# Optimization experiments

Measured on AMD Instinct MI355X. Metric: run time of the kernel, lower is better.

Reference implementation:

```python
import jax, jax.numpy as jnp
import numpy as np

BSZ, L, H, P = 4, 4096, 1024, 512
DT_MIN, DT_MAX = 1e-3, 1e-1


def setup_inputs() -> dict:
    key = jax.random.key(0)
    ks = jax.random.split(key, 6)
    input_sequence = jax.random.normal(ks[0], (BSZ, 1, H, 1, L), jnp.float32)
    # hidden_state_method='zero': hiddens arg only has to carry the right shape
    hiddens = jnp.zeros((BSZ, 1, P), jnp.float32)
    # stable (left-half-plane) diagonal state matrix, like HiPPO-LegS eigenvalues
    Lambda_re = -0.5 * jax.random.uniform(ks[1], (P,), jnp.float32) - 0.1
    Lambda_im = jnp.pi * jnp.arange(P, dtype=jnp.float32)
    # B stored as (P, H, 2) real/imag pair (lecun-ish scale), C as (H, P, 2)
    B = jax.random.normal(ks[2], (P, H, 2), jnp.float32) / jnp.sqrt(2.0 * H)
    C = jax.random.normal(ks[3], (H, P, 2), jnp.float32) / jnp.sqrt(2.0 * P)
    D = jax.random.normal(ks[4], (H,), jnp.float32)
    log_step = jax.random.uniform(ks[5], (P, 1), jnp.float32,
                                  minval=float(np.log(DT_MIN)),
                                  maxval=float(np.log(DT_MAX)))
    return dict(input_sequence=input_sequence, hiddens=hiddens,
                Lambda_re=Lambda_re, Lambda_im=Lambda_im,
                B=B, C=C, D=D, log_step=log_step)


def _binop(qi, qj):
    # diagonal linear recurrence combine: x_j = A_j * x_i + b_j
    Ai, bi = qi
    Aj, bj = qj
    return (Aj * Ai, Aj * bi + bj)


def _s5_forward(input_sequence, Lambda_re, Lambda_im, B, C, D, log_step):
    Lam = jax.lax.complex(Lambda_re, Lambda_im)              # (P,)
    step = jnp.exp(log_step[:, 0])                           # (P,)
    # zero-order-hold discretization
    Lambda_bar = jnp.exp(Lam * step)                         # (P,) complex
    B_scale = (Lambda_bar - 1.0) / Lam                       # (P,) complex
    B_bar_re = B_scale.real[:, None] * B[..., 0] - B_scale.imag[:, None] * B[..., 1]
    B_bar_im = B_scale.real[:, None] * B[..., 1] + B_scale.imag[:, None] * B[..., 0]

    u = input_sequence[:, 0, :, 0].transpose(0, 2, 1)        # (BSZ, L, H) float32

    # Bu_t = B_bar @ u_t, done on real/imag parts to keep u real in the GEMM
    Bu = jax.lax.complex(jnp.einsum('blh,ph->blp', u, B_bar_re),
                         jnp.einsum('blh,ph->blp', u, B_bar_im))  # (BSZ,L,P)
    # prepend zero hidden state (hidden_state_method='zero')
    zeros0 = jnp.zeros((Bu.shape[0], 1, Bu.shape[2]), Bu.dtype)
    Bu_elems = jnp.concatenate([zeros0, Bu], axis=1)          # (BSZ,L+1,P)
    Lam_elems = jnp.broadcast_to(Lambda_bar, Bu_elems.shape)  # (BSZ,L+1,P)

    _, xs = jax.lax.associative_scan(_binop, (Lam_elems, Bu_elems), axis=1)
    xs = xs[:, 1:]                                            # (BSZ,L,P) complex states

    # conj_sym=True: y_t = 2 * Re(C_tilde @ x_t)
    Cr, Ci = C[..., 0], C[..., 1]                             # (H,P) each
    ys = 2.0 * (jnp.einsum('hp,blp->blh', Cr, xs.real)
                - jnp.einsum('hp,blp->blh', Ci, xs.imag))     # (BSZ,L,H)
    ys = ys + D * u                                           # feedthrough
    ys = jax.nn.gelu(ys, approximate=False)                   # activation='gelu'
    return ys.transpose(0, 2, 1)[:, None, :, None, :]         # (BSZ,1,H,1,L)


def reference(input_sequence, hiddens, Lambda_re, Lambda_im, B, C, D, log_step):
    del hiddens  # unused with hidden_state_method='zero'
    return _s5_forward(input_sequence, Lambda_re, Lambda_im, B, C, D, log_step)
```

## Files before the change

### kernel.cpp

```cpp
#include <hip/hip_runtime.h>
#include <math.h>


constexpr int kB = 4, kL = 4096, kH = 1024, kP = 512;
constexpr int kM = 1024, kK = 1024, kN = 4096;

typedef short bf16x8 __attribute__((ext_vector_type(8)));
typedef float f32x4 __attribute__((ext_vector_type(4)));

constexpr size_t A1H_OFF = 0;
constexpr size_t A2H_OFF = A1H_OFF + (size_t)kM * kK * 2;
constexpr size_t LBAR_B  = A2H_OFF + (size_t)kM * kK * 2;
constexpr size_t BU_B    = (LBAR_B + 4096 + 255) & ~(size_t)255;
constexpr size_t TH_B    = BU_B + (size_t)kB * kM * kN * 4;
constexpr size_t MID_BYTES = TH_B + (size_t)kB * kN * kK * 2;

__device__ __forceinline__ unsigned short f2bf(float x) {
  unsigned int u = __float_as_uint(x);
  u += 0x7fffu + ((u >> 16) & 1u);
  return (unsigned short)(u >> 16);
}
__device__ __forceinline__ float bf2f(unsigned short h) {
  return __uint_as_float(((unsigned int)h) << 16);
}

__device__ __forceinline__ void gl2lds16(const void* g, void* l) {
  __builtin_amdgcn_global_load_lds(
      (const __attribute__((address_space(1))) void*)g,
      (__attribute__((address_space(3))) void*)l, 16, 0, 0);
}

template <int N>
__device__ __forceinline__ void wait_vm() {
  __builtin_amdgcn_s_waitcnt((N & 15) | ((N >> 4) << 14) | (15 << 8) | (7 << 4));
}

__global__ __launch_bounds__(256) void k_prep1(
    const float* __restrict__ Lre, const float* __restrict__ Lim,
    const float* __restrict__ B, const float* __restrict__ log_step,
    unsigned char* __restrict__ ws) {
  int p = blockIdx.x;
  float lr = Lre[p], li = Lim[p];
  float step = expf(log_step[p]);
  float er = expf(lr * step);
  float sb, cb;
  sincosf(li * step, &sb, &cb);
  float lbr = er * cb, lbi = er * sb;
  float nr = lbr - 1.0f, ni = lbi;
  float inv = 1.0f / (lr * lr + li * li);
  float sr = (nr * lr + ni * li) * inv;
  float si = (ni * lr - nr * li) * inv;

  if (threadIdx.x == 0) ((float2*)(ws + LBAR_B))[p] = make_float2(lbr, lbi);

  unsigned short* a1h = (unsigned short*)(ws + A1H_OFF);
  const float* Brow = B + (size_t)p * kH * 2;
  for (int h = threadIdx.x; h < kH; h += 256) {
    float br = Brow[2 * h], bi = Brow[2 * h + 1];
    a1h[(size_t)p * kK + h] = f2bf(sr * br - si * bi);
    a1h[(size_t)(kP + p) * kK + h] = f2bf(sr * bi + si * br);
  }
}

__global__ __launch_bounds__(256) void k_prep2(
    const float* __restrict__ C, unsigned char* __restrict__ ws) {
  int h = blockIdx.x;
  unsigned short* a2h = (unsigned short*)(ws + A2H_OFF);
  for (int k = threadIdx.x; k < kK; k += 256) {
    float v = (k < kP) ? 2.f * C[((size_t)h * kP + k) * 2]
                       : -2.f * C[((size_t)h * kP + (k - kP)) * 2 + 1];
    a2h[(size_t)h * kK + k] = f2bf(v);
  }
}

__global__ __launch_bounds__(256) void k_transpose(
    const float* __restrict__ in, unsigned short* __restrict__ oh) {
  __shared__ float t[64][65];
  int b = blockIdx.z;
  int r0 = blockIdx.y * 64;
  int c0 = blockIdx.x * 64;
  int tid = threadIdx.x;
  const float* src = in + ((size_t)b * 1024 + r0) * 4096 + c0;
  int cc = (tid & 15) * 4, rr = tid >> 4;
#pragma unroll
  for (int i = 0; i < 4; i++) {
    float4 v = *(const float4*)(src + (size_t)(rr + i * 16) * 4096 + cc);
    t[rr + i * 16][cc + 0] = v.x;
    t[rr + i * 16][cc + 1] = v.y;
    t[rr + i * 16][cc + 2] = v.z;
    t[rr + i * 16][cc + 3] = v.w;
  }
  __syncthreads();
  int oc = tid >> 2;
  int og = (tid & 3) * 2;
#pragma unroll
  for (int i = 0; i < 2; i++) {
    int g = og + i;
    unsigned short hv[8];
#pragma unroll
    for (int j = 0; j < 8; j++) hv[j] = f2bf(t[g * 8 + j][oc]);
    size_t ob = ((size_t)b * 4096 + c0 + oc) * 1024 + r0 + g * 8;
    *(uint4*)(oh + ob) = *(uint4*)hv;
  }
}


__device__ __forceinline__ int stage_src_off(int Dp) {
  int Ds = Dp ^ (((Dp >> 9) & 1) << 5);
  int s = Ds >> 10, d = Ds & 1023;
  int row = ((s >> 1) << 4) + (d >> 6);
  int kk = ((s & 1) << 5) + ((d & 63) >> 1);
  return row * kK + kk;
}

__device__ __forceinline__ void stg_half(const unsigned short* p, int h, int kt,
                                         unsigned char* lds, int lbase,
                                         int rowk0, int rowk1, int d0, int d1) {
  const unsigned short* s = p + (size_t)h * (128 * kK) + kt * 64;
  gl2lds16(s + rowk0, lds + lbase + h * 16384 + d0);
  gl2lds16(s + rowk1, lds + lbase + h * 16384 + d1);
}

template <int MH>
__device__ __forceinline__ void rd_ah(bf16x8 (&a)[4][2], const unsigned char* lds,
                                      int base, int wmrb, int lane_off) {
#pragma unroll
  for (int mi = 0; mi < 4; mi++)
#pragma unroll
    for (int ks = 0; ks < 2; ks++)
      a[mi][ks] = *(const bf16x8*)(lds + base +
          (((wmrb + MH * 4 + mi) * 2 + ks) << 10) + lane_off);
}
template <int NH>
__device__ __forceinline__ void rd_bh(bf16x8 (&bb)[2][2][2], const unsigned char* lds,
                                      int base, int wnrb, int lane_off) {
#pragma unroll
  for (int nj = 0; nj < 2; nj++)
#pragma unroll
    for (int ks = 0; ks < 2; ks++)
      bb[NH][nj][ks] = *(const bf16x8*)(lds + base +
          (((wnrb + NH * 2 + nj) * 2 + ks) << 10) + lane_off);
}

template <int MH, int NH>
__device__ __forceinline__ void mfma_quad(f32x4 (&acc)[8][4], bf16x8 (&a)[4][2],
                                          bf16x8 (&bb)[2][2][2]) {
  __builtin_amdgcn_s_setprio(1);
#pragma unroll
  for (int ks = 0; ks < 2; ks++)
#pragma unroll
    for (int mi = 0; mi < 4; mi++)
#pragma unroll
      for (int nj = 0; nj < 2; nj++)
        acc[MH * 4 + mi][NH * 2 + nj] = __builtin_amdgcn_mfma_f32_16x16x32_bf16(
            a[mi][ks], bb[NH][nj][ks], acc[MH * 4 + mi][NH * 2 + nj], 0, 0, 0);
  __builtin_amdgcn_s_setprio(0);
}

#define BAR __builtin_amdgcn_s_barrier()
#define LGKM0                                           \
  do {                                                  \
    asm volatile("s_waitcnt lgkmcnt(0)" ::: "memory");  \
    __builtin_amdgcn_sched_barrier(0);                  \
  } while (0)

template <bool EPI>
__global__ __launch_bounds__(512) void k_gemm8(
    const unsigned short* __restrict__ Ah, const unsigned short* __restrict__ Bh,
    float* __restrict__ out, const float* __restrict__ u,
    const float* __restrict__ D) {
  __shared__ __align__(16) unsigned char lds[131072];
  constexpr int LA0 = 0, LA1 = 32768, LB0 = 65536, LB1 = 98304;
  constexpr int NT2 = kK / 128;

  int b = blockIdx.z;
  int m0 = blockIdx.y * 256, n0 = blockIdx.x * 256;
  int tid = threadIdx.x, w = tid >> 6;
  int q = (tid >> 4) & 3, r = tid & 15;
  int wm = (w >> 2) * 128, wn = (w & 3) * 64;
  int wmrb = (w >> 2) * 8, wnrb = (w & 3) * 4;
  int lane_off = (r * 64 + q * 16) ^ ((r & 8) << 2);

  int d0 = tid << 4, d1 = 8192 + (tid << 4);
  int rowk0 = stage_src_off(d0), rowk1 = stage_src_off(d1);

  const unsigned short* pA = Ah + (size_t)m0 * kK;
  const unsigned short* pB = Bh + (size_t)b * kN * kK + (size_t)n0 * kK;

  f32x4 acc[8][4] = {};
  bf16x8 a[4][2], bb[2][2][2];

#define STG(P, H, KT, LB) stg_half(P, H, KT, lds, LB, rowk0, rowk1, d0, d1)

  STG(pA, 0, 0, LA0); STG(pA, 1, 0, LA0);
  STG(pB, 0, 0, LB0); STG(pB, 1, 0, LB0);
  STG(pB, 0, 1, LB1); STG(pB, 1, 1, LB1);
  wait_vm<4>();
  BAR;

  for (int it = 0; it < NT2; ++it) {
    int kt = it * 2;
    bool pf = (it + 1 < NT2);
    rd_ah<0>(a, lds, LA0, wmrb, lane_off);
    rd_bh<0>(bb, lds, LB0, wnrb, lane_off);
    STG(pA, 0, kt + 1, LA1);
    BAR; LGKM0; mfma_quad<0, 0>(acc, a, bb); BAR;
    rd_bh<1>(bb, lds, LB0, wnrb, lane_off);
    STG(pA, 1, kt + 1, LA1);
    BAR; LGKM0; mfma_quad<0, 1>(acc, a, bb); BAR;
    rd_ah<1>(a, lds, LA0, wmrb, lane_off);
    if (pf) STG(pB, 0, kt + 2, LB0);
    BAR; LGKM0; mfma_quad<1, 1>(acc, a, bb); BAR;
    if (pf) STG(pB, 1, kt + 2, LB0);
    BAR; mfma_quad<1, 0>(acc, a, bb);
    if (pf) wait_vm<4>(); else wait_vm<0>();
    BAR;
    rd_ah<0>(a, lds, LA1, wmrb, lane_off);
    rd_bh<0>(bb, lds, LB1, wnrb, lane_off);
    if (pf) STG(pA, 0, kt + 2, LA0);
    BAR; LGKM0; mfma_quad<0, 0>(acc, a, bb); BAR;
    rd_bh<1>(bb, lds, LB1, wnrb, lane_off);
    if (pf) STG(pA, 1, kt + 2, LA0);
    BAR; LGKM0; mfma_quad<0, 1>(acc, a, bb); BAR;
    rd_ah<1>(a, lds, LA1, wmrb, lane_off);
    if (pf) STG(pB, 0, kt + 3, LB1);
    BAR; LGKM0; mfma_quad<1, 1>(acc, a, bb); BAR;
    if (pf) STG(pB, 1, kt + 3, LB1);
    BAR; mfma_quad<1, 0>(acc, a, bb);
    if (pf) wait_vm<4>();
    BAR;
  }
#undef STG

#pragma unroll
  for (int mi = 0; mi < 8; mi++) {
#pragma unroll
    for (int reg = 0; reg < 4; reg++) {
      int row = m0 + wm + mi * 16 + q * 4 + reg;
      float dv = EPI ? D[row] : 0.f;
#pragma unroll
      for (int ni = 0; ni < 4; ni++) {
        int col = n0 + wn + ni * 16 + r;
        size_t o = ((size_t)b * kM + row) * (size_t)kN + col;
        float v = acc[mi][ni][reg];
        if (EPI) {
          float y = v + dv * u[o];
          v = 0.5f * y * (1.f + erff(y * 0.70710678118654752f));
        }
        out[o] = v;
      }
    }
  }
}

__global__ __launch_bounds__(256) void k_scan(float* __restrict__ bu,
                                              const float2* __restrict__ lbar) {
  int p = blockIdx.x & (kP - 1);
  int b = blockIdx.x >> 9;
  int tid = threadIdx.x, lane = tid & 63, w = tid >> 6;
  float2 lam = lbar[p];
  float* sre = bu + ((size_t)b * kM + p) * (size_t)kN;
  float* sim = sre + (size_t)kP * kN;

  float vr[16], vi[16];
  {
    const float4* pr = (const float4*)(sre + tid * 16);
    const float4* pi = (const float4*)(sim + tid * 16);
#pragma unroll
    for (int i = 0; i < 4; i++) {
      float4 a = pr[i], c = pi[i];
      vr[4 * i] = a.x; vr[4 * i + 1] = a.y; vr[4 * i + 2] = a.z; vr[4 * i + 3] = a.w;
      vi[4 * i] = c.x; vi[4 * i + 1] = c.y; vi[4 * i + 2] = c.z; vi[4 * i + 3] = c.w;
    }
  }

  float xr = 0.f, xi = 0.f;
#pragma unroll
  for (int i = 0; i < 16; i++) {
    float nr2 = fmaf(lam.x, xr, fmaf(-lam.y, xi, vr[i]));
    float ni2 = fmaf(lam.x, xi, fmaf(lam.y, xr, vi[i]));
    xr = nr2; xi = ni2;
  }

  float Ar = lam.x, Ai = lam.y;
#pragma unroll
  for (int s = 0; s < 4; s++) {
    float tr = Ar * Ar - Ai * Ai, ti = 2.f * Ar * Ai;
    Ar = tr; Ai = ti;
  }
  float br = xr, bi = xi;

  for (int off = 1; off < 64; off <<= 1) {
    float pAr = __shfl_up(Ar, off), pAi = __shfl_up(Ai, off);
    float pbr = __shfl_up(br, off), pbi = __shfl_up(bi, off);
    if (lane >= off) {
      float nAr = Ar * pAr - Ai * pAi;
      float nAi = Ar * pAi + Ai * pAr;
      float nbr = Ar * pbr - Ai * pbi + br;
      float nbi = Ar * pbi + Ai * pbr + bi;
      Ar = nAr; Ai = nAi; br = nbr; bi = nbi;
    }
  }

  __shared__ float4 wtot[4];
  if (lane == 63) wtot[w] = make_float4(Ar, Ai, br, bi);
  __syncthreads();

  float eAr = __shfl_up(Ar, 1), eAi = __shfl_up(Ai, 1);
  float ebr = __shfl_up(br, 1), ebi = __shfl_up(bi, 1);
  if (lane == 0) { eAr = 1.f; eAi = 0.f; ebr = 0.f; ebi = 0.f; }

  float pAr = 1.f, pAi = 0.f, pbr = 0.f, pbi = 0.f;
  for (int j = 0; j < w; j++) {
    float4 t = wtot[j];
    float nAr = t.x * pAr - t.y * pAi;
    float nAi = t.x * pAi + t.y * pAr;
    float nbr = t.x * pbr - t.y * pbi + t.z;
    float nbi = t.x * pbi + t.y * pbr + t.w;
    pAr = nAr; pAi = nAi; pbr = nbr; pbi = nbi;
  }

  float initr = eAr * pbr - eAi * pbi + ebr;
  float initi = eAr * pbi + eAi * pbr + ebi;

  xr = initr; xi = initi;
  float4* qr = (float4*)(sre + tid * 16);
  float4* qi = (float4*)(sim + tid * 16);
#pragma unroll
  for (int i = 0; i < 4; i++) {
    float rr[4], ii[4];
#pragma unroll
    for (int j = 0; j < 4; j++) {
      float nr2 = fmaf(lam.x, xr, fmaf(-lam.y, xi, vr[4 * i + j]));
      float ni2 = fmaf(lam.x, xi, fmaf(lam.y, xr, vi[4 * i + j]));
      xr = nr2; xi = ni2; rr[j] = nr2; ii[j] = ni2;
    }
    qr[i] = make_float4(rr[0], rr[1], rr[2], rr[3]);
    qi[i] = make_float4(ii[0], ii[1], ii[2], ii[3]);
  }
}

constexpr size_t OBBAR = 0;
constexpr size_t OLBAR = (size_t)kP * kH;
constexpr size_t OBU = OLBAR + 1024;

__global__ __launch_bounds__(256) void k_precomputeF(
    const float* __restrict__ Lre, const float* __restrict__ Lim,
    const float* __restrict__ B, const float* __restrict__ log_step,
    float2* __restrict__ ws) {
  int p = blockIdx.x;
  float lr = Lre[p], li = Lim[p];
  float step = expf(log_step[p]);
  float er = expf(lr * step);
  float sb, cb;
  sincosf(li * step, &sb, &cb);
  float lbr = er * cb, lbi = er * sb;
  float nr = lbr - 1.0f, ni = lbi;
  float inv = 1.0f / (lr * lr + li * li);
  float sr = (nr * lr + ni * li) * inv;
  float si = (ni * lr - nr * li) * inv;
  if (threadIdx.x == 0) ws[OLBAR + p] = make_float2(lbr, lbi);
  float2* Bbar = ws + OBBAR;
  const float* Brow = B + (size_t)p * kH * 2;
  for (int h = threadIdx.x; h < kH; h += 256) {
    float br = Brow[2 * h], bi = Brow[2 * h + 1];
    Bbar[(size_t)p * kH + h] = make_float2(sr * br - si * bi, sr * bi + si * br);
  }
}

__global__ __launch_bounds__(256) void k_gemm1F(
    const float2* __restrict__ ws_bbar, const float* __restrict__ u,
    float2* __restrict__ Bu) {
  __shared__ float2 As[16][64];
  __shared__ float Bs[16][64];
  int b = blockIdx.z, m0 = blockIdx.y * 64, n0 = blockIdx.x * 64;
  int tid = threadIdx.x, tn = tid & 15, tm = tid >> 4;
  const float* uB = u + (size_t)b * kH * kL;
  float2 acc[4][4];
#pragma unroll
  for (int i = 0; i < 4; i++)
#pragma unroll
    for (int j = 0; j < 4; j++) acc[i][j] = make_float2(0.f, 0.f);
  int ar = tid >> 2, ac = (tid & 3) * 4, bk = tid >> 4, bc = (tid & 15) * 4;
  for (int k0 = 0; k0 < kH; k0 += 16) {
    const float4* src = (const float4*)(ws_bbar + (size_t)(m0 + ar) * kH + k0 + ac);
    float4 v01 = src[0], v23 = src[1];
    As[ac + 0][ar] = make_float2(v01.x, v01.y);
    As[ac + 1][ar] = make_float2(v01.z, v01.w);
    As[ac + 2][ar] = make_float2(v23.x, v23.y);
    As[ac + 3][ar] = make_float2(v23.z, v23.w);
    float4 v = *(const float4*)(uB + (size_t)(k0 + bk) * kL + n0 + bc);
    *(float4*)&Bs[bk][bc] = v;
    __syncthreads();
#pragma unroll
    for (int kk = 0; kk < 16; ++kk) {
      const float4* arow = (const float4*)&As[kk][0];
      float4 a01 = arow[tm * 2 + 0], a23 = arow[tm * 2 + 1];
      float2 a[4] = {make_float2(a01.x, a01.y), make_float2(a01.z, a01.w),
                     make_float2(a23.x, a23.y), make_float2(a23.z, a23.w)};
      float4 bv = ((const float4*)&Bs[kk][0])[tn];
      float bbv[4] = {bv.x, bv.y, bv.z, bv.w};
#pragma unroll
      for (int mi = 0; mi < 4; mi++)
#pragma unroll
        for (int ni = 0; ni < 4; ni++) {
          acc[mi][ni].x = fmaf(a[mi].x, bbv[ni], acc[mi][ni].x);
          acc[mi][ni].y = fmaf(a[mi].y, bbv[ni], acc[mi][ni].y);
        }
    }
    __syncthreads();
  }
  float2* BuB = Bu + (size_t)b * kP * kL;
#pragma unroll
  for (int mi = 0; mi < 4; mi++) {
    int row = m0 + tm * 4 + mi;
    float2* dst = BuB + (size_t)row * kL + n0 + tn * 4;
    ((float4*)dst)[0] = make_float4(acc[mi][0].x, acc[mi][0].y, acc[mi][1].x, acc[mi][1].y);
    ((float4*)dst)[1] = make_float4(acc[mi][2].x, acc[mi][2].y, acc[mi][3].x, acc[mi][3].y);
  }
}

__global__ __launch_bounds__(256) void k_scanF(float2* __restrict__ Bu,
                                               const float2* __restrict__ Lbar) {
  int p = blockIdx.x & (kP - 1);
  int b = blockIdx.x >> 9;
  int tid = threadIdx.x, lane = tid & 63, w = tid >> 6;
  float2 lam = Lbar[p];
  float2* seq = Bu + ((size_t)b * kP + p) * kL;
  float2 v[16];
  const float4* src = (const float4*)(seq + tid * 16);
#pragma unroll
  for (int i = 0; i < 8; i++) {
    float4 t = src[i];
    v[2 * i] = make_float2(t.x, t.y);
    v[2 * i + 1] = make_float2(t.z, t.w);
  }
  float xr = 0.f, xi = 0.f;
#pragma unroll
  for (int i = 0; i < 16; i++) {
    float nr2 = fmaf(lam.x, xr, fmaf(-lam.y, xi, v[i].x));
    float ni2 = fmaf(lam.x, xi, fmaf(lam.y, xr, v[i].y));
    xr = nr2; xi = ni2;
  }
  float Ar = lam.x, Ai = lam.y;
#pragma unroll
  for (int s = 0; s < 4; s++) {
    float tr = Ar * Ar - Ai * Ai, ti = 2.f * Ar * Ai;
    Ar = tr; Ai = ti;
  }
  float br = xr, bi = xi;
  for (int off = 1; off < 64; off <<= 1) {
    float pAr = __shfl_up(Ar, off), pAi = __shfl_up(Ai, off);
    float pbr = __shfl_up(br, off), pbi = __shfl_up(bi, off);
    if (lane >= off) {
      float nAr = Ar * pAr - Ai * pAi, nAi = Ar * pAi + Ai * pAr;
      float nbr = Ar * pbr - Ai * pbi + br, nbi = Ar * pbi + Ai * pbr + bi;
      Ar = nAr; Ai = nAi; br = nbr; bi = nbi;
    }
  }
  __shared__ float4 wtot[4];
  if (lane == 63) wtot[w] = make_float4(Ar, Ai, br, bi);
  __syncthreads();
  float eAr = __shfl_up(Ar, 1), eAi = __shfl_up(Ai, 1);
  float ebr = __shfl_up(br, 1), ebi = __shfl_up(bi, 1);
  if (lane == 0) { eAr = 1.f; eAi = 0.f; ebr = 0.f; ebi = 0.f; }
  float pAr = 1.f, pAi = 0.f, pbr = 0.f, pbi = 0.f;
  for (int j = 0; j < w; j++) {
    float4 t = wtot[j];
    float nAr = t.x * pAr - t.y * pAi, nAi = t.x * pAi + t.y * pAr;
    float nbr = t.x * pbr - t.y * pbi + t.z, nbi = t.x * pbi + t.y * pbr + t.w;
    pAr = nAr; pAi = nAi; pbr = nbr; pbi = nbi;
  }
  float initr = eAr * pbr - eAi * pbi + ebr;
  float initi = eAr * pbi + eAi * pbr + ebi;
  xr = initr; xi = initi;
  float4* dst = (float4*)(seq + tid * 16);
#pragma unroll
  for (int i = 0; i < 8; i++) {
    float nr0 = fmaf(lam.x, xr, fmaf(-lam.y, xi, v[2 * i].x));
    float ni0 = fmaf(lam.x, xi, fmaf(lam.y, xr, v[2 * i].y));
    float nr1 = fmaf(lam.x, nr0, fmaf(-lam.y, ni0, v[2 * i + 1].x));
    float ni1 = fmaf(lam.x, ni0, fmaf(lam.y, nr0, v[2 * i + 1].y));
    dst[i] = make_float4(nr0, ni0, nr1, ni1);
    xr = nr1; xi = ni1;
  }
}

__global__ __launch_bounds__(256) void k_gemm2F(
    const float2* __restrict__ C, const float2* __restrict__ X,
    const float* __restrict__ u, const float* __restrict__ D,
    float* __restrict__ out) {
  __shared__ float2 As[16][64];
  __shared__ float2 Bs[16][64];
  int b = blockIdx.z, m0 = blockIdx.y * 64, n0 = blockIdx.x * 64;
  int tid = threadIdx.x, tn = tid & 15, tm = tid >> 4;
  const float2* Xb = X + (size_t)b * kP * kL;
  float acc[4][4];
#pragma unroll
  for (int i = 0; i < 4; i++)
#pragma unroll
    for (int j = 0; j < 4; j++) acc[i][j] = 0.f;
  int ar = tid >> 2, ac = (tid & 3) * 4, bk = tid >> 4, bc = (tid & 15) * 4;
  for (int k0 = 0; k0 < kP; k0 += 16) {
    const float4* src = (const float4*)(C + (size_t)(m0 + ar) * kP + k0 + ac);
    float4 v01 = src[0], v23 = src[1];
    As[ac + 0][ar] = make_float2(v01.x, v01.y);
    As[ac + 1][ar] = make_float2(v01.z, v01.w);
    As[ac + 2][ar] = make_float2(v23.x, v23.y);
    As[ac + 3][ar] = make_float2(v23.z, v23.w);
    const float4* srcb = (const float4*)(Xb + (size_t)(k0 + bk) * kL + n0 + bc);
    ((float4*)&Bs[bk][bc])[0] = srcb[0];
    ((float4*)&Bs[bk][bc])[1] = srcb[1];
    __syncthreads();
#pragma unroll
    for (int kk = 0; kk < 16; ++kk) {
      const float4* arow = (const float4*)&As[kk][0];
      float4 a01 = arow[tm * 2 + 0], a23 = arow[tm * 2 + 1];
      float2 a[4] = {make_float2(a01.x, a01.y), make_float2(a01.z, a01.w),
                     make_float2(a23.x, a23.y), make_float2(a23.z, a23.w)};
      const float4* brow = (const float4*)&Bs[kk][0];
      float4 b01 = brow[tn * 2 + 0], b23 = brow[tn * 2 + 1];
      float2 bbv[4] = {make_float2(b01.x, b01.y), make_float2(b01.z, b01.w),
                       make_float2(b23.x, b23.y), make_float2(b23.z, b23.w)};
#pragma unroll
      for (int mi = 0; mi < 4; mi++)
#pragma unroll
        for (int ni = 0; ni < 4; ni++) {
          acc[mi][ni] = fmaf(a[mi].x, bbv[ni].x, acc[mi][ni]);
          acc[mi][ni] = fmaf(-a[mi].y, bbv[ni].y, acc[mi][ni]);
        }
    }
    __syncthreads();
  }
#pragma unroll
  for (int mi = 0; mi < 4; mi++) {
    int h = m0 + tm * 4 + mi;
    float d = D[h];
    const float* urow = u + ((size_t)b * kH + h) * kL + n0 + tn * 4;
    float4 uv = *(const float4*)urow;
    float uu[4] = {uv.x, uv.y, uv.z, uv.w};
    float res[4];
#pragma unroll
    for (int ni = 0; ni < 4; ni++) {
      float y = 2.f * acc[mi][ni] + d * uu[ni];
      res[ni] = 0.5f * y * (1.f + erff(y * 0.70710678118654752f));
    }
    float* orow = out + ((size_t)b * kH + h) * kL + n0 + tn * 4;
    *(float4*)orow = make_float4(res[0], res[1], res[2], res[3]);
  }
}

extern "C" void kernel_launch(void* const* d_in, const int* in_sizes, int n_in,
                              void* d_out, int out_size, void* d_ws, size_t ws_size,
                              hipStream_t stream) {
  const float* input_sequence = (const float*)d_in[0];
  const float* Lambda_re = (const float*)d_in[2];
  const float* Lambda_im = (const float*)d_in[3];
  const float* B = (const float*)d_in[4];
  const float* C = (const float*)d_in[5];
  const float* D = (const float*)d_in[6];
  const float* log_step = (const float*)d_in[7];
  float* out = (float*)d_out;

  if (ws_size >= MID_BYTES) {
    unsigned char* ws = (unsigned char*)d_ws;
    unsigned short* a1h = (unsigned short*)(ws + A1H_OFF);
    unsigned short* a2h = (unsigned short*)(ws + A2H_OFF);
    float2* lbar = (float2*)(ws + LBAR_B);
    float* bu = (float*)(ws + BU_B);
    unsigned short* th = (unsigned short*)(ws + TH_B);

    k_prep1<<<dim3(kP), 256, 0, stream>>>(Lambda_re, Lambda_im, B, log_step, ws);
    k_prep2<<<dim3(kH), 256, 0, stream>>>(C, ws);

    dim3 tgrid(kL / 64, 1024 / 64, kB);
    dim3 ggrid(kN / 256, kM / 256, kB);

    k_transpose<<<tgrid, 256, 0, stream>>>(input_sequence, th);
    k_gemm8<false><<<ggrid, 512, 0, stream>>>(a1h, th, bu, nullptr, nullptr);
    k_scan<<<dim3(kB * kP), 256, 0, stream>>>(bu, lbar);
    k_transpose<<<tgrid, 256, 0, stream>>>(bu, th);
    k_gemm8<true><<<ggrid, 512, 0, stream>>>(a2h, th, out, input_sequence, D);
  } else {
    float2* ws = (float2*)d_ws;
    float2* Bbar = ws + OBBAR;
    float2* Lbar = ws + OLBAR;
    float2* Bu = ws + OBU;
    k_precomputeF<<<dim3(kP), 256, 0, stream>>>(Lambda_re, Lambda_im, B, log_step, ws);
    k_gemm1F<<<dim3(kL / 64, kP / 64, kB), 256, 0, stream>>>(Bbar, input_sequence, Bu);
    k_scanF<<<dim3(kB * kP), 256, 0, stream>>>(Bu, Lbar);
    k_gemm2F<<<dim3(kL / 64, kH / 64, kB), 256, 0, stream>>>(
        (const float2*)C, (const float2*)Bu, input_sequence, D, out);
  }
}
```

Before: 294.7 us.

## Shrink GEMM tiles to 128x256 with K-step 32 for higher occupancy

Replaces the 256x256, K-step 64 bf16 MFMA GEMM with a 128x256 tile and K-step 32. LDS use drops from 128KB to 48KB and the accumulators from 8x4 to 4x4 fragments, and launch_bounds now asks for multiple blocks per CU. The aim is to let more waves run per CU and to double the grid for better load balance. In exchange, each block reuses its data less, issues more loop iterations and barriers per unit of work, and reads more from global memory.

```diff
diff --git a/kernel.cpp b/kernel.cpp
--- a/kernel.cpp
+++ b/kernel.cpp
@@ -105,55 +105,39 @@
 }
 
 
-__device__ __forceinline__ int stage_src_off(int Dp) {
+__device__ __forceinline__ int stage_src_off32(int Dp) {
   int Ds = Dp ^ (((Dp >> 9) & 1) << 5);
   int s = Ds >> 10, d = Ds & 1023;
-  int row = ((s >> 1) << 4) + (d >> 6);
-  int kk = ((s & 1) << 5) + ((d & 63) >> 1);
+  int row = (s << 4) + (d >> 6);
+  int kk = (d & 63) >> 1;
   return row * kK + kk;
 }
 
-__device__ __forceinline__ void stg_half(const unsigned short* p, int h, int kt,
-                                         unsigned char* lds, int lbase,
-                                         int rowk0, int rowk1, int d0, int d1) {
-  const unsigned short* s = p + (size_t)h * (128 * kK) + kt * 64;
-  gl2lds16(s + rowk0, lds + lbase + h * 16384 + d0);
-  gl2lds16(s + rowk1, lds + lbase + h * 16384 + d1);
-}
-
 template <int MH>
-__device__ __forceinline__ void rd_ah(bf16x8 (&a)[4][2], const unsigned char* lds,
+__device__ __forceinline__ void rd_a2(bf16x8 (&a)[2], const unsigned char* lds,
                                       int base, int wmrb, int lane_off) {
 #pragma unroll
-  for (int mi = 0; mi < 4; mi++)
-#pragma unroll
-    for (int ks = 0; ks < 2; ks++)
-      a[mi][ks] = *(const bf16x8*)(lds + base +
-          (((wmrb + MH * 4 + mi) * 2 + ks) << 10) + lane_off);
+  for (int i = 0; i < 2; i++)
+    a[i] = *(const bf16x8*)(lds + base + ((wmrb + MH * 2 + i) << 10) + lane_off);
 }
 template <int NH>
-__device__ __forceinline__ void rd_bh(bf16x8 (&bb)[2][2][2], const unsigned char* lds,
+__device__ __forceinline__ void rd_b2(bf16x8 (&bb)[2][2], const unsigned char* lds,
                                       int base, int wnrb, int lane_off) {
 #pragma unroll
-  for (int nj = 0; nj < 2; nj++)
-#pragma unroll
-    for (int ks = 0; ks < 2; ks++)
-      bb[NH][nj][ks] = *(const bf16x8*)(lds + base +
-          (((wnrb + NH * 2 + nj) * 2 + ks) << 10) + lane_off);
+  for (int i = 0; i < 2; i++)
+    bb[NH][i] = *(const bf16x8*)(lds + base + ((wnrb + NH * 2 + i) << 10) + lane_off);
 }
 
 template <int MH, int NH>
-__device__ __forceinline__ void mfma_quad(f32x4 (&acc)[8][4], bf16x8 (&a)[4][2],
-                                          bf16x8 (&bb)[2][2][2]) {
+__device__ __forceinline__ void quad4(f32x4 (&acc)[4][4], bf16x8 (&a)[2],
+                                      bf16x8 (&bb)[2][2]) {
   __builtin_amdgcn_s_setprio(1);
 #pragma unroll
-  for (int ks = 0; ks < 2; ks++)
-#pragma unroll
-    for (int mi = 0; mi < 4; mi++)
-#pragma unroll
-      for (int nj = 0; nj < 2; nj++)
-        acc[MH * 4 + mi][NH * 2 + nj] = __builtin_amdgcn_mfma_f32_16x16x32_bf16(
-            a[mi][ks], bb[NH][nj][ks], acc[MH * 4 + mi][NH * 2 + nj], 0, 0, 0);
+  for (int mi = 0; mi < 2; mi++)
+#pragma unroll
+    for (int nj = 0; nj < 2; nj++)
+      acc[MH * 2 + mi][NH * 2 + nj] = __builtin_amdgcn_mfma_f32_16x16x32_bf16(
+          a[mi], bb[NH][nj], acc[MH * 2 + mi][NH * 2 + nj], 0, 0, 0);
   __builtin_amdgcn_s_setprio(0);
 }
 
@@ -165,75 +149,78 @@
   } while (0)
 
 template <bool EPI>
-__global__ __launch_bounds__(512) void k_gemm8(
+__global__ __launch_bounds__(512, 4) void k_gemm32(
     const unsigned short* __restrict__ Ah, const unsigned short* __restrict__ Bh,
     float* __restrict__ out, const float* __restrict__ u,
     const float* __restrict__ D) {
-  __shared__ __align__(16) unsigned char lds[131072];
-  constexpr int LA0 = 0, LA1 = 32768, LB0 = 65536, LB1 = 98304;
-  constexpr int NT2 = kK / 128;
+  __shared__ __align__(16) unsigned char lds[49152];
+  constexpr int LA0 = 0, LA1 = 8192, LB0 = 16384, LB1 = 32768;
+  constexpr int NT2 = kK / 64;
 
   int b = blockIdx.z;
-  int m0 = blockIdx.y * 256, n0 = blockIdx.x * 256;
+  int m0 = blockIdx.y * 128, n0 = blockIdx.x * 256;
   int tid = threadIdx.x, w = tid >> 6;
   int q = (tid >> 4) & 3, r = tid & 15;
-  int wm = (w >> 2) * 128, wn = (w & 3) * 64;
-  int wmrb = (w >> 2) * 8, wnrb = (w & 3) * 4;
+  int wm = (w >> 2) * 64, wn = (w & 3) * 64;
+  int wmrb = (w >> 2) * 4, wnrb = (w & 3) * 4;
   int lane_off = (r * 64 + q * 16) ^ ((r & 8) << 2);
 
-  int d0 = tid << 4, d1 = 8192 + (tid << 4);
-  int rowk0 = stage_src_off(d0), rowk1 = stage_src_off(d1);
+  int d0 = tid << 4;
+  int rowk = stage_src_off32(d0);
 
   const unsigned short* pA = Ah + (size_t)m0 * kK;
   const unsigned short* pB = Bh + (size_t)b * kN * kK + (size_t)n0 * kK;
 
-  f32x4 acc[8][4] = {};
-  bf16x8 a[4][2], bb[2][2][2];
-
-#define STG(P, H, KT, LB) stg_half(P, H, KT, lds, LB, rowk0, rowk1, d0, d1)
-
-  STG(pA, 0, 0, LA0); STG(pA, 1, 0, LA0);
-  STG(pB, 0, 0, LB0); STG(pB, 1, 0, LB0);
-  STG(pB, 0, 1, LB1); STG(pB, 1, 1, LB1);
-  wait_vm<4>();
+  f32x4 acc[4][4] = {};
+  bf16x8 a[2], bb[2][2];
+
+#define STG_A(KT, LB)                                             \
+  gl2lds16(pA + (KT) * 32 + rowk, lds + (LB) + d0)
+#define STG_B(H, KT, LB)                                          \
+  gl2lds16(pB + (size_t)(H) * 128 * kK + (KT) * 32 + rowk,        \
+           lds + (LB) + (H) * 8192 + d0)
+
+  STG_A(0, LA0);
+  STG_B(0, 0, LB0); STG_B(1, 0, LB0);
+  STG_B(0, 1, LB1); STG_B(1, 1, LB1);
+  wait_vm<2>();
   BAR;
 
   for (int it = 0; it < NT2; ++it) {
     int kt = it * 2;
     bool pf = (it + 1 < NT2);
-    rd_ah<0>(a, lds, LA0, wmrb, lane_off);
-    rd_bh<0>(bb, lds, LB0, wnrb, lane_off);
-    STG(pA, 0, kt + 1, LA1);
-    BAR; LGKM0; mfma_quad<0, 0>(acc, a, bb); BAR;
-    rd_bh<1>(bb, lds, LB0, wnrb, lane_off);
-    STG(pA, 1, kt + 1, LA1);
-    BAR; LGKM0; mfma_quad<0, 1>(acc, a, bb); BAR;
-    rd_ah<1>(a, lds, LA0, wmrb, lane_off);
-    if (pf) STG(pB, 0, kt + 2, LB0);
-    BAR; LGKM0; mfma_quad<1, 1>(acc, a, bb); BAR;
-    if (pf) STG(pB, 1, kt + 2, LB0);
-    BAR; mfma_quad<1, 0>(acc, a, bb);
-    if (pf) wait_vm<4>(); else wait_vm<0>();
+    rd_a2<0>(a, lds, LA0, wmrb, lane_off);
+    rd_b2<0>(bb, lds, LB0, wnrb, lane_off);
+    STG_A(kt + 1, LA1);
+    BAR; LGKM0; quad4<0, 0>(acc, a, bb); BAR;
+    rd_b2<1>(bb, lds, LB0, wnrb, lane_off);
+    BAR; LGKM0; quad4<0, 1>(acc, a, bb); BAR;
+    rd_a2<1>(a, lds, LA0, wmrb, lane_off);
+    if (pf) STG_B(0, kt + 2, LB0);
+    BAR; LGKM0; quad4<1, 1>(acc, a, bb); BAR;
+    if (pf) STG_B(1, kt + 2, LB0);
+    BAR; quad4<1, 0>(acc, a, bb);
+    if (pf) wait_vm<2>(); else wait_vm<0>();
     BAR;
-    rd_ah<0>(a, lds, LA1, wmrb, lane_off);
-    rd_bh<0>(bb, lds, LB1, wnrb, lane_off);
-    if (pf) STG(pA, 0, kt + 2, LA0);
-    BAR; LGKM0; mfma_quad<0, 0>(acc, a, bb); BAR;
-    rd_bh<1>(bb, lds, LB1, wnrb, lane_off);
-    if (pf) STG(pA, 1, kt + 2, LA0);
-    BAR; LGKM0; mfma_quad<0, 1>(acc, a, bb); BAR;
-    rd_ah<1>(a, lds, LA1, wmrb, lane_off);
-    if (pf) STG(pB, 0, kt + 3, LB1);
-    BAR; LGKM0; mfma_quad<1, 1>(acc, a, bb); BAR;
-    if (pf) STG(pB, 1, kt + 3, LB1);
-    BAR; mfma_quad<1, 0>(acc, a, bb);
-    if (pf) wait_vm<4>();
+    rd_a2<0>(a, lds, LA1, wmrb, lane_off);
+    rd_b2<0>(bb, lds, LB1, wnrb, lane_off);
+    if (pf) STG_A(kt + 2, LA0);
+    BAR; LGKM0; quad4<0, 0>(acc, a, bb); BAR;
+    rd_b2<1>(bb, lds, LB1, wnrb, lane_off);
+    BAR; LGKM0; quad4<0, 1>(acc, a, bb); BAR;
+    rd_a2<1>(a, lds, LA1, wmrb, lane_off);
+    if (pf) STG_B(0, kt + 3, LB1);
+    BAR; LGKM0; quad4<1, 1>(acc, a, bb); BAR;
+    if (pf) STG_B(1, kt + 3, LB1);
+    BAR; quad4<1, 0>(acc, a, bb);
+    if (pf) wait_vm<2>();
     BAR;
   }
-#undef STG
-
-#pragma unroll
-  for (int mi = 0; mi < 8; mi++) {
+#undef STG_A
+#undef STG_B
+
+#pragma unroll
+  for (int mi = 0; mi < 4; mi++) {
 #pragma unroll
     for (int reg = 0; reg < 4; reg++) {
       int row = m0 + wm + mi * 16 + q * 4 + reg;
@@ -574,13 +561,13 @@
     k_prep2<<<dim3(kH), 256, 0, stream>>>(C, ws);
 
     dim3 tgrid(kL / 64, 1024 / 64, kB);
-    dim3 ggrid(kN / 256, kM / 256, kB);
+    dim3 ggrid(kN / 256, kM / 128, kB);
 
     k_transpose<<<tgrid, 256, 0, stream>>>(input_sequence, th);
-    k_gemm8<false><<<ggrid, 512, 0, stream>>>(a1h, th, bu, nullptr, nullptr);
+    k_gemm32<false><<<ggrid, 512, 0, stream>>>(a1h, th, bu, nullptr, nullptr);
     k_scan<<<dim3(kB * kP), 256, 0, stream>>>(bu, lbar);
     k_transpose<<<tgrid, 256, 0, stream>>>(bu, th);
-    k_gemm8<true><<<ggrid, 512, 0, stream>>>(a2h, th, out, input_sequence, D);
+    k_gemm32<true><<<ggrid, 512, 0, stream>>>(a2h, th, out, input_sequence, D);
   } else {
     float2* ws = (float2*)d_ws;
     float2* Bbar = ws + OBBAR;
```

Result: no change. 291.1 us (-1.2%).
